# Optimization experiments

Hardware: AMD Instinct MI355X
Metric: run time of the kernel (lower is better)

## Reference

```python
import jax, jax.numpy as jnp
import numpy as np

S, N, A = 64, 4096, 32
HID, DM, NH, DK = 256, 128, 4, 32
EPS = 1e-5
SCALE = float(np.sqrt(DK))


def setup_inputs() -> dict:
    key = jax.random.key(0)
    ks = jax.random.split(key, 20)
    w = lambda i, sh: jax.random.normal(ks[i], sh, jnp.float32) * 0.02
    z = lambda n: jnp.zeros((n,), jnp.float32)
    return {
        "agent_states": jax.random.normal(ks[0], (N, S), jnp.float32),
        "sw1": w(1, (N * S, HID)), "sb1": z(HID),
        "sw2": w(2, (HID, HID)), "sb2": z(HID),
        "sow": w(3, (HID, 64)), "sob": z(64),
        "tw": w(4, (S + 64, DM)), "tb": z(DM),
        "wq": w(5, (DM, DM)), "bq": z(DM),
        "wk": w(6, (DM, DM)), "bk": z(DM),
        "wv": w(7, (DM, DM)), "bv": z(DM),
        "wo": w(8, (DM, DM)), "bo": z(DM),
        "ln_g": jnp.ones((DM,), jnp.float32), "ln_b": z(DM),
        "taw1": w(9, (DM, 64)), "tab1": z(64),
        "taw2": w(10, (64, 32)), "tab2": z(32),
        "ow1": w(11, (S + DM + 32, 256)), "ob1": z(256),
        "ow2": w(12, (256, DM)), "ob2": z(DM),
        "aw": w(13, (DM, A)), "ab": z(A),
        "vw": w(14, (DM, 1)), "vb": z(1),
        "cw": w(15, (S, 64)), "cb": z(64),
        "cdw": w(16, (64, 32)), "cdb": z(32),
    }


def reference(agent_states, sw1, sb1, sw2, sb2, sow, sob, tw, tb,
              wq, bq, wk, bk, wv, bv, wo, bo, ln_g, ln_b,
              taw1, tab1, taw2, tab2, ow1, ob1, ow2, ob2,
              aw, ab, vw, vb, cw, cb, cdw, cdb):
    n = agent_states.shape[0]
    # strategic level: flatten all agent states -> global objective [64]
    gs = agent_states.reshape(-1)
    strat = jax.nn.relu(jax.nn.relu(gs @ sw1 + sb1) @ sw2 + sb2)
    gobj = strat @ sow + sob
    # tactical encode (batched over agents instead of Python loop)
    tact_in = jnp.concatenate(
        [agent_states, jnp.broadcast_to(gobj, (n, gobj.shape[0]))], axis=-1)
    tact = jax.nn.relu(tact_in @ tw + tb)[None]  # [1, n, DM]
    # multi-head attention across agents
    q = (tact @ wq + bq).reshape(1, n, NH, DK).transpose(0, 2, 1, 3)
    k = (tact @ wk + bk).reshape(1, n, NH, DK).transpose(0, 2, 1, 3)
    v = (tact @ wv + bv).reshape(1, n, NH, DK).transpose(0, 2, 1, 3)
    scores = jnp.einsum('bhqd,bhkd->bhqk', q, k) / SCALE
    attn = jax.nn.softmax(scores, axis=-1)  # [1, NH, n, n]
    ctx = jnp.einsum('bhqk,bhkd->bhqd', attn, v).transpose(0, 2, 1, 3).reshape(1, n, DM)
    res = ctx @ wo + bo + tact
    mu = res.mean(-1, keepdims=True)
    var = res.var(-1, keepdims=True)  # biased, like torch LayerNorm
    coord = ((res - mu) / jnp.sqrt(var + EPS) * ln_g + ln_b)[0]  # [n, DM]
    # task allocation (softmax over 32 tasks)
    task = jax.nn.softmax(jax.nn.relu(coord @ taw1 + tab1) @ taw2 + tab2, axis=-1)
    # operational level -> actions / values
    op_in = jnp.concatenate([agent_states, coord, task], axis=-1)
    opf = jax.nn.relu(jax.nn.relu(op_in @ ow1 + ob1) @ ow2 + ob2)
    actions = opf @ aw + ab
    values = opf @ vw + vb
    # communication messages (two stacked linears, no activation in source)
    messages = (agent_states @ cw + cb) @ cdw + cdb
    return actions, values, messages, task, attn, gobj
```

## Files before the change

kernel.cpp:

```cpp
#include <hip/hip_runtime.h>

typedef __attribute__((ext_vector_type(8))) short s8v;
typedef __attribute__((ext_vector_type(4))) short s4v;
typedef __attribute__((ext_vector_type(4))) float f4v;

#define MFMA16(a, b, c) __builtin_amdgcn_mfma_f32_16x16x32_bf16((a), (b), (c), 0, 0, 0)

#define NAG   4096
#define SDIM  64
#define DMOD  128
#define NHD   4
#define DKD   32
#define HIDD  256
static constexpr float INV_SCALE = 0.17677669529663687f;
static constexpr float EPSV = 1e-5f;

#define OFF_ACT   0
#define OFF_VAL   131072
#define OFF_MSG   135168
#define OFF_TASK  266240
#define OFF_ATTN  397312
#define OFF_GOBJ  67506176

static constexpr size_t WS_P1   = 0;
static constexpr size_t WS_P1B  = 524288;
static constexpr size_t WS_P2   = 540672;
static constexpr size_t WS_TACT = 558080;
static constexpr size_t WS_Q    = 2655232;
static constexpr size_t WS_K    = 3703808;
static constexpr size_t WS_VT   = 4752384;
static constexpr size_t WS_CTX  = 5800960;
static constexpr size_t WS_OPIN = 7898112;
static constexpr size_t WS_H    = 9733120;
static constexpr size_t WS_OPF  = 11830272;
static constexpr size_t WS_OW1T = 12878848;
static constexpr size_t WS_OW2T = 12993536;

typedef unsigned short u16;
typedef unsigned int   u32;

static __device__ __forceinline__ u16 f2bf(float f) {
    union { float f; u32 u; } x; x.f = f;
    u32 r = x.u + 0x7FFFu + ((x.u >> 16) & 1u);
    return (u16)(r >> 16);
}
static __device__ __forceinline__ float bf2f(u16 b) {
    union { u32 u; float f; } x; x.u = ((u32)b) << 16;
    return x.f;
}

__global__ __launch_bounds__(256) void k1_sw1(const float* __restrict__ gs,
                                              const float* __restrict__ sw1,
                                              float* __restrict__ p1,
                                              const float* __restrict__ ow1,
                                              const float* __restrict__ ow2,
                                              u16* __restrict__ w1t,
                                              u16* __restrict__ w2t) {
    int tid = threadIdx.x;
    int b = blockIdx.x;
    if (b >= 512) {
        int bb = b - 512;
        if (bb < 224) {
            w1t[tid * 224 + bb] = f2bf(ow1[bb * 256 + tid]);
        } else if (tid < 128) {
            int k0 = (bb - 224) * 8;
#pragma unroll
            for (int kk = 0; kk < 8; ++kk) {
                int k = k0 + kk;
                w2t[tid * 256 + k] = f2bf(ow2[k * 128 + tid]);
            }
        }
        return;
    }
    __shared__ float gsl[512];
    __shared__ float red[4][256];
    gsl[tid]       = gs[b * 512 + tid];
    gsl[tid + 256] = gs[b * 512 + 256 + tid];
    __syncthreads();
    int t = tid & 63;
    int rg = tid >> 6;
    const f4v* w4 = (const f4v*)sw1;
    f4v acc = {0.f, 0.f, 0.f, 0.f};
    size_t rb = (size_t)b * 512;
#pragma unroll 4
    for (int r = rg; r < 512; r += 4) {
        float g = gsl[r];
        f4v w = __builtin_nontemporal_load(&w4[(rb + r) * 64 + t]);
        acc[0] += g * w[0]; acc[1] += g * w[1]; acc[2] += g * w[2]; acc[3] += g * w[3];
    }
    red[rg][4 * t + 0] = acc[0]; red[rg][4 * t + 1] = acc[1];
    red[rg][4 * t + 2] = acc[2]; red[rg][4 * t + 3] = acc[3];
    __syncthreads();
    float s = red[0][tid] + red[1][tid] + red[2][tid] + red[3][tid];
    p1[b * 256 + tid] = s;
}

__global__ void k1b_red(const float* __restrict__ p1, float* __restrict__ p1b) {
    int j = threadIdx.x;
    int b0 = blockIdx.x * 32;
    float s = 0.f;
#pragma unroll
    for (int b = 0; b < 32; ++b) s += p1[(b0 + b) * 256 + j];
    p1b[blockIdx.x * 256 + j] = s;
}

__global__ void k2b_strat(const float* __restrict__ p1b, const float* __restrict__ sb1,
                          const float* __restrict__ sw2, float* __restrict__ p2) {
    __shared__ float h1[256];
    int j = threadIdx.x;
    float s = 0.f;
#pragma unroll
    for (int b = 0; b < 16; ++b) s += p1b[b * 256 + j];
    h1[j] = fmaxf(s + sb1[j], 0.f);
    __syncthreads();
    int i0 = blockIdx.x * 16;
    float acc = 0.f;
#pragma unroll
    for (int i = 0; i < 16; ++i) acc += h1[i0 + i] * sw2[(i0 + i) * 256 + j];
    p2[blockIdx.x * 256 + j] = acc;
}

__global__ __launch_bounds__(256) void k3_tact_qkv(
    const float* __restrict__ p2, const float* __restrict__ sb2,
    const float* __restrict__ sow, const float* __restrict__ sob,
    const float* __restrict__ as, const float* __restrict__ tw, const float* __restrict__ tb,
    const float* __restrict__ wq, const float* __restrict__ bq,
    const float* __restrict__ wk, const float* __restrict__ bk,
    const float* __restrict__ wv, const float* __restrict__ bv,
    float* __restrict__ out_gobj, float* __restrict__ tactws,
    u16* __restrict__ qws, u16* __restrict__ kws, u16* __restrict__ vtws) {
    __shared__ float strat[256];
    __shared__ float gobj[64];
    __shared__ float asl[8][64];
    __shared__ float tl[8][128];
    int tid = threadIdx.x;
    int a0 = blockIdx.x * 8;
    {
        float s = 0.f;
#pragma unroll
        for (int b = 0; b < 16; ++b) s += p2[b * 256 + tid];
        strat[tid] = fmaxf(s + sb2[tid], 0.f);
    }
#pragma unroll
    for (int r = 0; r < 2; ++r) {
        int idx = tid + r * 256;
        asl[idx >> 6][idx & 63] = as[a0 * 64 + idx];
    }
    __syncthreads();
    if (tid < 64) {
        float g = sob[tid];
        for (int i = 0; i < 256; ++i) g += strat[i] * sow[i * 64 + tid];
        gobj[tid] = g;
        if (blockIdx.x == 0) out_gobj[tid] = g;
    }
    __syncthreads();
    int ah = tid >> 7, j = tid & 127;
    float gacc = 0.f;
    for (int i = 0; i < 64; ++i) gacc += gobj[i] * tw[(64 + i) * 128 + j];
    float acc[4];
    float base = tb[j] + gacc;
#pragma unroll
    for (int a = 0; a < 4; ++a) acc[a] = base;
    for (int i = 0; i < 64; ++i) {
        float w = tw[i * 128 + j];
#pragma unroll
        for (int a = 0; a < 4; ++a) acc[a] += asl[ah * 4 + a][i] * w;
    }
#pragma unroll
    for (int a = 0; a < 4; ++a) {
        float t = fmaxf(acc[a], 0.f);
        tl[ah * 4 + a][j] = t;
        tactws[(size_t)(a0 + ah * 4 + a) * 128 + j] = t;
    }
    __syncthreads();
    int h = j >> 5, d = j & 31;
#pragma unroll
    for (int a = 0; a < 4; ++a) acc[a] = 0.f;
    for (int i = 0; i < 128; ++i) {
        float w = wq[i * 128 + j];
#pragma unroll
        for (int a = 0; a < 4; ++a) acc[a] += tl[ah * 4 + a][i] * w;
    }
#pragma unroll
    for (int a = 0; a < 4; ++a)
        qws[h * 131072 + (a0 + ah * 4 + a) * 32 + d] = f2bf((acc[a] + bq[j]) * INV_SCALE);
#pragma unroll
    for (int a = 0; a < 4; ++a) acc[a] = 0.f;
    for (int i = 0; i < 128; ++i) {
        float w = wk[i * 128 + j];
#pragma unroll
        for (int a = 0; a < 4; ++a) acc[a] += tl[ah * 4 + a][i] * w;
    }
#pragma unroll
    for (int a = 0; a < 4; ++a)
        kws[h * 131072 + (a0 + ah * 4 + a) * 32 + d] = f2bf(acc[a] + bk[j]);
#pragma unroll
    for (int a = 0; a < 4; ++a) acc[a] = 0.f;
    for (int i = 0; i < 128; ++i) {
        float w = wv[i * 128 + j];
#pragma unroll
        for (int a = 0; a < 4; ++a) acc[a] += tl[ah * 4 + a][i] * w;
    }
    union { u16 u[4]; s4v v; } pk;
#pragma unroll
    for (int a = 0; a < 4; ++a) pk.u[a] = f2bf(acc[a] + bv[j]);
    *(s4v*)(vtws + h * 131072 + d * 4096 + a0 + ah * 4) = pk.v;
}

__global__ __launch_bounds__(512) void k4_attn(
    const u16* __restrict__ qws, const u16* __restrict__ kws, const u16* __restrict__ vtws,
    float* __restrict__ attn, float* __restrict__ ctxws) {
    int tid = threadIdx.x;
    int wid = tid >> 6;
    int l = tid & 63;
    int g = l >> 4;
    int ln = l & 15;
    int h = blockIdx.x >> 8;
    int qt = (blockIdx.x & 255) * 16;
    const u16* qh = qws + h * 131072;
    const u16* kh = kws + h * 131072;
    const u16* vh = vtws + h * 131072;
    int j0 = wid * 512;

    s8v aq = *(const s8v*)(qh + (qt + ln) * 32 + 8 * g);
    f4v zero = {0.f, 0.f, 0.f, 0.f};

    __shared__ __align__(16) union SmemU {
        struct {
            float red[8][16];
            u16 ldsPb[8][2][16][40];
            float pctx[8][16][32];
        } a;
        float sT[2][16][260];
    } sm;

    f4v lacc = zero, accA = zero, accB = zero;
    int buf = 0;
    for (int jc = 0; jc < 16; ++jc) {
        int jb = j0 + jc * 32;
        s8v b0 = *(const s8v*)(kh + (jb + ln) * 32 + 8 * g);
        s8v b1 = *(const s8v*)(kh + (jb + 16 + ln) * 32 + 8 * g);
        f4v S0 = MFMA16(aq, b0, zero);
        f4v S1 = MFMA16(aq, b1, zero);
#pragma unroll
        for (int r = 0; r < 4; ++r) {
            float w0 = __expf(S0[r]);
            float w1 = __expf(S1[r]);
            lacc[r] += w0 + w1;
            sm.a.ldsPb[wid][buf][4 * g + r][ln] = f2bf(w0);
            sm.a.ldsPb[wid][buf][4 * g + r][16 + ln] = f2bf(w1);
        }
        s8v bp = *(const s8v*)&sm.a.ldsPb[wid][buf][ln][8 * g];
        s8v va = *(const s8v*)(vh + ln * 4096 + jb + 8 * g);
        s8v vb = *(const s8v*)(vh + (16 + ln) * 4096 + jb + 8 * g);
        accA = MFMA16(va, bp, accA);
        accB = MFMA16(vb, bp, accB);
        buf ^= 1;
    }
#pragma unroll
    for (int m = 1; m <= 8; m <<= 1) {
        lacc[0] += __shfl_xor(lacc[0], m);
        lacc[1] += __shfl_xor(lacc[1], m);
        lacc[2] += __shfl_xor(lacc[2], m);
        lacc[3] += __shfl_xor(lacc[3], m);
    }
    if (ln == 0) {
#pragma unroll
        for (int r = 0; r < 4; ++r) sm.a.red[wid][4 * g + r] = lacc[r];
    }
    __syncthreads();
    float linvq = 1.f / (sm.a.red[0][ln] + sm.a.red[1][ln] + sm.a.red[2][ln] + sm.a.red[3][ln] +
                         sm.a.red[4][ln] + sm.a.red[5][ln] + sm.a.red[6][ln] + sm.a.red[7][ln]);
#pragma unroll
    for (int r = 0; r < 4; ++r) {
        sm.a.pctx[wid][ln][4 * g + r] = accA[r] * linvq;
        sm.a.pctx[wid][ln][16 + 4 * g + r] = accB[r] * linvq;
    }
    __syncthreads();
    {
        int q = tid >> 5;
        int d = tid & 31;
        float s = sm.a.pctx[0][q][d] + sm.a.pctx[1][q][d] + sm.a.pctx[2][q][d] + sm.a.pctx[3][q][d] +
                  sm.a.pctx[4][q][d] + sm.a.pctx[5][q][d] + sm.a.pctx[6][q][d] + sm.a.pctx[7][q][d];
        ctxws[(size_t)(qt + q) * 128 + h * 32 + d] = s;
    }
    __syncthreads();

    float* attnh = attn + (size_t)h * 4096 * 4096;
    auto COMPUTE = [&](int c, int p) {
        int co = wid * 32;
        int jb = c * 256 + co;
        s8v b0 = *(const s8v*)(kh + (jb + ln) * 32 + 8 * g);
        s8v b1 = *(const s8v*)(kh + (jb + 16 + ln) * 32 + 8 * g);
        f4v S0 = MFMA16(b0, aq, zero);
        f4v S1 = MFMA16(b1, aq, zero);
        f4v o0, o1;
#pragma unroll
        for (int r = 0; r < 4; ++r) {
            o0[r] = __expf(S0[r]) * linvq;
            o1[r] = __expf(S1[r]) * linvq;
        }
        *(f4v*)&sm.sT[p][ln][co + 4 * g] = o0;
        *(f4v*)&sm.sT[p][ln][co + 16 + 4 * g] = o1;
    };
    auto STORE = [&](int c, int p) {
#pragma unroll
        for (int r2 = 0; r2 < 2; ++r2) {
            int row = 2 * wid + r2;
            f4v t = *(const f4v*)&sm.sT[p][row][4 * l];
            *(f4v*)(attnh + (size_t)(qt + row) * 4096 + c * 256 + 4 * l) = t;
        }
    };
    COMPUTE(0, 0);
    __syncthreads();
    for (int c = 1; c < 16; ++c) {
        STORE(c - 1, (c - 1) & 1);
        COMPUTE(c, c & 1);
        __syncthreads();
    }
    STORE(15, 1);
}

__global__ __launch_bounds__(512) void k5_post(
    const float* __restrict__ ctxws, const float* __restrict__ tactws,
    const float* __restrict__ wo, const float* __restrict__ bo,
    const float* __restrict__ lng, const float* __restrict__ lnb,
    const float* __restrict__ taw1, const float* __restrict__ tab1,
    const float* __restrict__ taw2, const float* __restrict__ tab2,
    const float* __restrict__ as, float* __restrict__ dout, u16* __restrict__ opin) {
    __shared__ float wos[128 * 128];
    __shared__ float tw1s[128 * 64];
    __shared__ float tw2s[64 * 32];
    __shared__ float cx[8][128];
    __shared__ float coords[8][128];
    __shared__ float t1v[8][64];
    int tid = threadIdx.x;
    for (int i = tid; i < 128 * 128; i += 512) wos[i] = wo[i];
    for (int i = tid; i < 128 * 64; i += 512) tw1s[i] = taw1[i];
    for (int i = tid; i < 64 * 32; i += 512) tw2s[i] = taw2[i];
    __syncthreads();
    int w = tid >> 6, l = tid & 63;
    for (int it = 0; it < 2; ++it) {
        int n = blockIdx.x * 16 + w * 2 + it;
        float c0 = ctxws[(size_t)n * 128 + l], c1 = ctxws[(size_t)n * 128 + 64 + l];
        float t0 = tactws[(size_t)n * 128 + l], t1 = tactws[(size_t)n * 128 + 64 + l];
        float av = as[n * 64 + l];
        cx[w][l] = c0; cx[w][64 + l] = c1;
        __syncthreads();
        float r0 = bo[l] + t0, r1 = bo[64 + l] + t1;
        for (int k = 0; k < 128; ++k) {
            float cv = cx[w][k];
            r0 += cv * wos[k * 128 + l];
            r1 += cv * wos[k * 128 + 64 + l];
        }
        float s = r0 + r1;
#pragma unroll
        for (int m = 1; m <= 32; m <<= 1) s += __shfl_xor(s, m);
        float mu = s * (1.f / 128.f);
        float d0 = r0 - mu, d1 = r1 - mu;
        float vs = d0 * d0 + d1 * d1;
#pragma unroll
        for (int m = 1; m <= 32; m <<= 1) vs += __shfl_xor(vs, m);
        float rstd = 1.f / sqrtf(vs * (1.f / 128.f) + EPSV);
        float co0 = d0 * rstd * lng[l] + lnb[l];
        float co1 = d1 * rstd * lng[64 + l] + lnb[64 + l];
        coords[w][l] = co0; coords[w][64 + l] = co1;
        opin[(size_t)n * 224 + l] = f2bf(av);
        opin[(size_t)n * 224 + 64 + l] = f2bf(co0);
        opin[(size_t)n * 224 + 128 + l] = f2bf(co1);
        __syncthreads();
        float a1 = tab1[l];
        for (int i = 0; i < 128; ++i) a1 += coords[w][i] * tw1s[i * 64 + l];
        t1v[w][l] = fmaxf(a1, 0.f);
        __syncthreads();
        if (l < 32) {
            float a2 = tab2[l];
            for (int i = 0; i < 64; ++i) a2 += t1v[w][i] * tw2s[i * 32 + l];
            float mx = a2;
#pragma unroll
            for (int m = 1; m <= 16; m <<= 1) mx = fmaxf(mx, __shfl_xor(mx, m));
            float e = __expf(a2 - mx);
            float se = e;
#pragma unroll
            for (int m = 1; m <= 16; m <<= 1) se += __shfl_xor(se, m);
            float tk = e / se;
            dout[OFF_TASK + n * 32 + l] = tk;
            opin[(size_t)n * 224 + 192 + l] = f2bf(tk);
        }
        __syncthreads();
    }
}

__global__ __launch_bounds__(256) void k6a(const u16* __restrict__ opin, const u16* __restrict__ w1t,
                                           const float* __restrict__ ob1, u16* __restrict__ Hws) {
    int tid = threadIdx.x;
    int w = tid >> 6, l = tid & 63, g = l >> 4, ln = l & 15;
    int bm = blockIdx.x & 63, bn = blockIdx.x >> 6;
    int m0 = bm * 64 + w * 16, n0 = bn * 64;
    f4v acc[4];
    f4v zero = {0.f, 0.f, 0.f, 0.f};
#pragma unroll
    for (int nt = 0; nt < 4; ++nt) acc[nt] = zero;
    for (int kt = 0; kt < 7; ++kt) {
        s8v A = *(const s8v*)(opin + (size_t)(m0 + ln) * 224 + kt * 32 + 8 * g);
#pragma unroll
        for (int nt = 0; nt < 4; ++nt) {
            s8v B = *(const s8v*)(w1t + (size_t)(n0 + nt * 16 + ln) * 224 + kt * 32 + 8 * g);
            acc[nt] = MFMA16(A, B, acc[nt]);
        }
    }
#pragma unroll
    for (int nt = 0; nt < 4; ++nt) {
        int col = n0 + nt * 16 + ln;
        float bias = ob1[col];
#pragma unroll
        for (int r = 0; r < 4; ++r) {
            int row = m0 + 4 * g + r;
            Hws[(size_t)row * 256 + col] = f2bf(fmaxf(acc[nt][r] + bias, 0.f));
        }
    }
}

__global__ __launch_bounds__(256) void k6b(const u16* __restrict__ Hws, const u16* __restrict__ w2t,
                                           const float* __restrict__ ob2, u16* __restrict__ opfws) {
    int tid = threadIdx.x;
    int w = tid >> 6, l = tid & 63, g = l >> 4, ln = l & 15;
    int bm = blockIdx.x & 63, bn = blockIdx.x >> 6;
    int m0 = bm * 64 + w * 16, n0 = bn * 64;
    f4v acc[4];
    f4v zero = {0.f, 0.f, 0.f, 0.f};
#pragma unroll
    for (int nt = 0; nt < 4; ++nt) acc[nt] = zero;
    for (int kt = 0; kt < 8; ++kt) {
        s8v A = *(const s8v*)(Hws + (size_t)(m0 + ln) * 256 + kt * 32 + 8 * g);
#pragma unroll
        for (int nt = 0; nt < 4; ++nt) {
            s8v B = *(const s8v*)(w2t + (size_t)(n0 + nt * 16 + ln) * 256 + kt * 32 + 8 * g);
            acc[nt] = MFMA16(A, B, acc[nt]);
        }
    }
#pragma unroll
    for (int nt = 0; nt < 4; ++nt) {
        int col = n0 + nt * 16 + ln;
        float bias = ob2[col];
#pragma unroll
        for (int r = 0; r < 4; ++r) {
            int row = m0 + 4 * g + r;
            opfws[(size_t)row * 128 + col] = f2bf(fmaxf(acc[nt][r] + bias, 0.f));
        }
    }
}

__global__ __launch_bounds__(256) void k6c(const u16* __restrict__ opf, const float* __restrict__ as,
                                           const float* __restrict__ aw, const float* __restrict__ ab,
                                           const float* __restrict__ vw, const float* __restrict__ vb,
                                           const float* __restrict__ cw, const float* __restrict__ cb,
                                           const float* __restrict__ cdw, const float* __restrict__ cdb,
                                           float* __restrict__ dout) {
    __shared__ float opfs[4][128];
    __shared__ float asl[4][64];
    __shared__ float m1s[4][64];
    int tid = threadIdx.x;
    int w = tid >> 6, l = tid & 63;
    int n = blockIdx.x * 4 + w;
    {
        u32 u = *(const u32*)(opf + (size_t)n * 128 + 2 * l);
        opfs[w][2 * l] = bf2f((u16)(u & 0xffff));
        opfs[w][2 * l + 1] = bf2f((u16)(u >> 16));
        asl[w][l] = as[n * 64 + l];
    }
    __syncthreads();
    if (l < 32) {
        float a = ab[l];
        for (int k = 0; k < 128; ++k) a += opfs[w][k] * aw[k * 32 + l];
        dout[OFF_ACT + n * 32 + l] = a;
    }
    {
        float p = opfs[w][l] * vw[l] + opfs[w][64 + l] * vw[64 + l];
#pragma unroll
        for (int m = 1; m <= 32; m <<= 1) p += __shfl_xor(p, m);
        if (l == 0) dout[OFF_VAL + n] = p + vb[0];
    }
    {
        float a = cb[l];
        for (int k = 0; k < 64; ++k) a += asl[w][k] * cw[k * 64 + l];
        m1s[w][l] = a;
    }
    __syncthreads();
    if (l < 32) {
        float a = cdb[l];
        for (int k = 0; k < 64; ++k) a += m1s[w][k] * cdw[k * 32 + l];
        dout[OFF_MSG + n * 32 + l] = a;
    }
}

extern "C" void kernel_launch(void* const* d_in, const int* in_sizes, int n_in,
                              void* d_out, int out_size, void* d_ws, size_t ws_size,
                              hipStream_t stream) {
    const float* as  = (const float*)d_in[0];
    const float* sw1 = (const float*)d_in[1];
    const float* sb1 = (const float*)d_in[2];
    const float* sw2 = (const float*)d_in[3];
    const float* sb2 = (const float*)d_in[4];
    const float* sow = (const float*)d_in[5];
    const float* sob = (const float*)d_in[6];
    const float* tw  = (const float*)d_in[7];
    const float* tb  = (const float*)d_in[8];
    const float* wq  = (const float*)d_in[9];
    const float* bq  = (const float*)d_in[10];
    const float* wk  = (const float*)d_in[11];
    const float* bk  = (const float*)d_in[12];
    const float* wv  = (const float*)d_in[13];
    const float* bv  = (const float*)d_in[14];
    const float* wo  = (const float*)d_in[15];
    const float* bo  = (const float*)d_in[16];
    const float* lng = (const float*)d_in[17];
    const float* lnb = (const float*)d_in[18];
    const float* taw1 = (const float*)d_in[19];
    const float* tab1 = (const float*)d_in[20];
    const float* taw2 = (const float*)d_in[21];
    const float* tab2 = (const float*)d_in[22];
    const float* ow1 = (const float*)d_in[23];
    const float* ob1 = (const float*)d_in[24];
    const float* ow2 = (const float*)d_in[25];
    const float* ob2 = (const float*)d_in[26];
    const float* aw  = (const float*)d_in[27];
    const float* ab  = (const float*)d_in[28];
    const float* vw  = (const float*)d_in[29];
    const float* vb  = (const float*)d_in[30];
    const float* cw  = (const float*)d_in[31];
    const float* cb  = (const float*)d_in[32];
    const float* cdw = (const float*)d_in[33];
    const float* cdb = (const float*)d_in[34];

    float* dout = (float*)d_out;
    char* ws = (char*)d_ws;
    float* p1    = (float*)(ws + WS_P1);
    float* p1b   = (float*)(ws + WS_P1B);
    float* p2    = (float*)(ws + WS_P2);
    float* tactw = (float*)(ws + WS_TACT);
    u16*   qws   = (u16*)(ws + WS_Q);
    u16*   kws   = (u16*)(ws + WS_K);
    u16*   vtws  = (u16*)(ws + WS_VT);
    float* ctxws = (float*)(ws + WS_CTX);
    u16*   opin  = (u16*)(ws + WS_OPIN);
    u16*   Hws   = (u16*)(ws + WS_H);
    u16*   opfws = (u16*)(ws + WS_OPF);
    u16*   w1t   = (u16*)(ws + WS_OW1T);
    u16*   w2t   = (u16*)(ws + WS_OW2T);

    hipLaunchKernelGGL(k1_sw1, dim3(768), dim3(256), 0, stream, as, sw1, p1, ow1, ow2, w1t, w2t);
    hipLaunchKernelGGL(k1b_red, dim3(16), dim3(256), 0, stream, p1, p1b);
    hipLaunchKernelGGL(k2b_strat, dim3(16), dim3(256), 0, stream, p1b, sb1, sw2, p2);
    hipLaunchKernelGGL(k3_tact_qkv, dim3(512), dim3(256), 0, stream,
                       p2, sb2, sow, sob, as, tw, tb, wq, bq, wk, bk, wv, bv,
                       dout + OFF_GOBJ, tactw, qws, kws, vtws);
    hipLaunchKernelGGL(k4_attn, dim3(1024), dim3(512), 0, stream,
                       qws, kws, vtws, dout + OFF_ATTN, ctxws);
    hipLaunchKernelGGL(k5_post, dim3(256), dim3(512), 0, stream,
                       ctxws, tactw, wo, bo, lng, lnb, taw1, tab1, taw2, tab2, as, dout, opin);
    hipLaunchKernelGGL(k6a, dim3(256), dim3(256), 0, stream, opin, w1t, ob1, Hws);
    hipLaunchKernelGGL(k6b, dim3(128), dim3(256), 0, stream, Hws, w2t, ob2, opfws);
    hipLaunchKernelGGL(k6c, dim3(1024), dim3(256), 0, stream,
                       opfws, as, aw, ab, vw, vb, cw, cb, cdw, cdb, dout);
}
```

Measured before the change: 194.5 us.

## Fuse operational GEMM2 with action/value/message heads; drop LDS weight staging in k5

The second operational GEMM and the action, value and message head kernel are merged into one kernel. Each block now computes a full 64x128 opf tile, keeps it in shared memory as fp32, and runs register-blocked head matmuls on it. This removes the bf16 opf round-trip through global memory and one kernel launch, but cuts the grid to 64 blocks. Separately, k5_post no longer copies wo, taw1 and taw2 into about 96KB of shared memory. It reads them through the cache instead and drops block-wide barriers, since each wave only uses its own shared rows. That should raise occupancy and remove the per-block staging cost.

```diff
diff --git a/kernel.cpp b/kernel.cpp
--- a/kernel.cpp
+++ b/kernel.cpp
@@ -328,17 +328,10 @@
     const float* __restrict__ taw1, const float* __restrict__ tab1,
     const float* __restrict__ taw2, const float* __restrict__ tab2,
     const float* __restrict__ as, float* __restrict__ dout, u16* __restrict__ opin) {
-    __shared__ float wos[128 * 128];
-    __shared__ float tw1s[128 * 64];
-    __shared__ float tw2s[64 * 32];
     __shared__ float cx[8][128];
     __shared__ float coords[8][128];
     __shared__ float t1v[8][64];
     int tid = threadIdx.x;
-    for (int i = tid; i < 128 * 128; i += 512) wos[i] = wo[i];
-    for (int i = tid; i < 128 * 64; i += 512) tw1s[i] = taw1[i];
-    for (int i = tid; i < 64 * 32; i += 512) tw2s[i] = taw2[i];
-    __syncthreads();
     int w = tid >> 6, l = tid & 63;
     for (int it = 0; it < 2; ++it) {
         int n = blockIdx.x * 16 + w * 2 + it;
@@ -346,12 +339,11 @@
         float t0 = tactws[(size_t)n * 128 + l], t1 = tactws[(size_t)n * 128 + 64 + l];
         float av = as[n * 64 + l];
         cx[w][l] = c0; cx[w][64 + l] = c1;
-        __syncthreads();
         float r0 = bo[l] + t0, r1 = bo[64 + l] + t1;
         for (int k = 0; k < 128; ++k) {
             float cv = cx[w][k];
-            r0 += cv * wos[k * 128 + l];
-            r1 += cv * wos[k * 128 + 64 + l];
+            r0 += cv * wo[k * 128 + l];
+            r1 += cv * wo[k * 128 + 64 + l];
         }
         float s = r0 + r1;
 #pragma unroll
@@ -368,14 +360,12 @@
         opin[(size_t)n * 224 + l] = f2bf(av);
         opin[(size_t)n * 224 + 64 + l] = f2bf(co0);
         opin[(size_t)n * 224 + 128 + l] = f2bf(co1);
-        __syncthreads();
         float a1 = tab1[l];
-        for (int i = 0; i < 128; ++i) a1 += coords[w][i] * tw1s[i * 64 + l];
+        for (int i = 0; i < 128; ++i) a1 += coords[w][i] * taw1[i * 64 + l];
         t1v[w][l] = fmaxf(a1, 0.f);
-        __syncthreads();
         if (l < 32) {
             float a2 = tab2[l];
-            for (int i = 0; i < 64; ++i) a2 += t1v[w][i] * tw2s[i * 32 + l];
+            for (int i = 0; i < 64; ++i) a2 += t1v[w][i] * taw2[i * 32 + l];
             float mx = a2;
 #pragma unroll
             for (int m = 1; m <= 16; m <<= 1) mx = fmaxf(mx, __shfl_xor(mx, m));
@@ -387,7 +377,6 @@
             dout[OFF_TASK + n * 32 + l] = tk;
             opin[(size_t)n * 224 + 192 + l] = f2bf(tk);
         }
-        __syncthreads();
     }
 }
 
@@ -421,76 +410,92 @@
     }
 }
 
-__global__ __launch_bounds__(256) void k6b(const u16* __restrict__ Hws, const u16* __restrict__ w2t,
-                                           const float* __restrict__ ob2, u16* __restrict__ opfws) {
+__global__ __launch_bounds__(256) void k6bc(const u16* __restrict__ Hws, const u16* __restrict__ w2t,
+                                            const float* __restrict__ ob2, const float* __restrict__ as,
+                                            const float* __restrict__ aw, const float* __restrict__ ab,
+                                            const float* __restrict__ vw, const float* __restrict__ vb,
+                                            const float* __restrict__ cw, const float* __restrict__ cb,
+                                            const float* __restrict__ cdw, const float* __restrict__ cdb,
+                                            float* __restrict__ dout) {
+    __shared__ float opfs[64][128];
+    __shared__ float asl[64][64];
+    __shared__ float m1s[64][64];
     int tid = threadIdx.x;
     int w = tid >> 6, l = tid & 63, g = l >> 4, ln = l & 15;
-    int bm = blockIdx.x & 63, bn = blockIdx.x >> 6;
-    int m0 = bm * 64 + w * 16, n0 = bn * 64;
-    f4v acc[4];
+    int m0 = blockIdx.x * 64;
+    int mw = m0 + w * 16;
+    for (int i = tid; i < 64 * 64; i += 256) asl[i >> 6][i & 63] = as[m0 * 64 + i];
+    f4v acc[8];
     f4v zero = {0.f, 0.f, 0.f, 0.f};
 #pragma unroll
-    for (int nt = 0; nt < 4; ++nt) acc[nt] = zero;
+    for (int nt = 0; nt < 8; ++nt) acc[nt] = zero;
     for (int kt = 0; kt < 8; ++kt) {
-        s8v A = *(const s8v*)(Hws + (size_t)(m0 + ln) * 256 + kt * 32 + 8 * g);
-#pragma unroll
-        for (int nt = 0; nt < 4; ++nt) {
-            s8v B = *(const s8v*)(w2t + (size_t)(n0 + nt * 16 + ln) * 256 + kt * 32 + 8 * g);
+        s8v A = *(const s8v*)(Hws + (size_t)(mw + ln) * 256 + kt * 32 + 8 * g);
+#pragma unroll
+        for (int nt = 0; nt < 8; ++nt) {
+            s8v B = *(const s8v*)(w2t + (size_t)(nt * 16 + ln) * 256 + kt * 32 + 8 * g);
             acc[nt] = MFMA16(A, B, acc[nt]);
         }
     }
 #pragma unroll
-    for (int nt = 0; nt < 4; ++nt) {
-        int col = n0 + nt * 16 + ln;
+    for (int nt = 0; nt < 8; ++nt) {
+        int col = nt * 16 + ln;
         float bias = ob2[col];
 #pragma unroll
-        for (int r = 0; r < 4; ++r) {
-            int row = m0 + 4 * g + r;
-            opfws[(size_t)row * 128 + col] = f2bf(fmaxf(acc[nt][r] + bias, 0.f));
-        }
-    }
-}
-
-__global__ __launch_bounds__(256) void k6c(const u16* __restrict__ opf, const float* __restrict__ as,
-                                           const float* __restrict__ aw, const float* __restrict__ ab,
-                                           const float* __restrict__ vw, const float* __restrict__ vb,
-                                           const float* __restrict__ cw, const float* __restrict__ cb,
-                                           const float* __restrict__ cdw, const float* __restrict__ cdb,
-                                           float* __restrict__ dout) {
-    __shared__ float opfs[4][128];
-    __shared__ float asl[4][64];
-    __shared__ float m1s[4][64];
-    int tid = threadIdx.x;
-    int w = tid >> 6, l = tid & 63;
-    int n = blockIdx.x * 4 + w;
+        for (int r = 0; r < 4; ++r)
+            opfs[w * 16 + 4 * g + r][col] = fmaxf(acc[nt][r] + bias, 0.f);
+    }
+    __syncthreads();
     {
-        u32 u = *(const u32*)(opf + (size_t)n * 128 + 2 * l);
-        opfs[w][2 * l] = bf2f((u16)(u & 0xffff));
-        opfs[w][2 * l + 1] = bf2f((u16)(u >> 16));
-        asl[w][l] = as[n * 64 + l];
-    }
-    __syncthreads();
-    if (l < 32) {
-        float a = ab[l];
-        for (int k = 0; k < 128; ++k) a += opfs[w][k] * aw[k * 32 + l];
-        dout[OFF_ACT + n * 32 + l] = a;
+        int c = tid & 31;
+        int r0 = (tid >> 5) * 8;
+        float o[8];
+#pragma unroll
+        for (int r = 0; r < 8; ++r) o[r] = ab[c];
+        for (int k = 0; k < 128; ++k) {
+            float wv_ = aw[k * 32 + c];
+#pragma unroll
+            for (int r = 0; r < 8; ++r) o[r] += opfs[r0 + r][k] * wv_;
+        }
+#pragma unroll
+        for (int r = 0; r < 8; ++r) dout[OFF_ACT + (m0 + r0 + r) * 32 + c] = o[r];
     }
     {
-        float p = opfs[w][l] * vw[l] + opfs[w][64 + l] * vw[64 + l];
-#pragma unroll
-        for (int m = 1; m <= 32; m <<= 1) p += __shfl_xor(p, m);
-        if (l == 0) dout[OFF_VAL + n] = p + vb[0];
+        int r = tid >> 2, q = tid & 3;
+        float p = 0.f;
+        for (int k = q * 32; k < q * 32 + 32; ++k) p += opfs[r][k] * vw[k];
+        p += __shfl_xor(p, 1);
+        p += __shfl_xor(p, 2);
+        if (q == 0) dout[OFF_VAL + m0 + r] = p + vb[0];
     }
     {
-        float a = cb[l];
-        for (int k = 0; k < 64; ++k) a += asl[w][k] * cw[k * 64 + l];
-        m1s[w][l] = a;
-    }
-    __syncthreads();
-    if (l < 32) {
-        float a = cdb[l];
-        for (int k = 0; k < 64; ++k) a += m1s[w][k] * cdw[k * 32 + l];
-        dout[OFF_MSG + n * 32 + l] = a;
+        int j = tid & 63;
+        int r0 = (tid >> 6) * 16;
+        float mo[16];
+#pragma unroll
+        for (int r = 0; r < 16; ++r) mo[r] = cb[j];
+        for (int k = 0; k < 64; ++k) {
+            float wv_ = cw[k * 64 + j];
+#pragma unroll
+            for (int r = 0; r < 16; ++r) mo[r] += asl[r0 + r][k] * wv_;
+        }
+#pragma unroll
+        for (int r = 0; r < 16; ++r) m1s[r0 + r][j] = mo[r];
+    }
+    __syncthreads();
+    {
+        int c = tid & 31;
+        int r0 = (tid >> 5) * 8;
+        float o[8];
+#pragma unroll
+        for (int r = 0; r < 8; ++r) o[r] = cdb[c];
+        for (int k = 0; k < 64; ++k) {
+            float wv_ = cdw[k * 32 + c];
+#pragma unroll
+            for (int r = 0; r < 8; ++r) o[r] += m1s[r0 + r][k] * wv_;
+        }
+#pragma unroll
+        for (int r = 0; r < 8; ++r) dout[OFF_MSG + (m0 + r0 + r) * 32 + c] = o[r];
     }
 }
 
@@ -545,7 +550,6 @@
     float* ctxws = (float*)(ws + WS_CTX);
     u16*   opin  = (u16*)(ws + WS_OPIN);
     u16*   Hws   = (u16*)(ws + WS_H);
-    u16*   opfws = (u16*)(ws + WS_OPF);
     u16*   w1t   = (u16*)(ws + WS_OW1T);
     u16*   w2t   = (u16*)(ws + WS_OW2T);
 
@@ -560,7 +564,6 @@
     hipLaunchKernelGGL(k5_post, dim3(256), dim3(512), 0, stream,
                        ctxws, tactw, wo, bo, lng, lnb, taw1, tab1, taw2, tab2, as, dout, opin);
     hipLaunchKernelGGL(k6a, dim3(256), dim3(256), 0, stream, opin, w1t, ob1, Hws);
-    hipLaunchKernelGGL(k6b, dim3(128), dim3(256), 0, stream, Hws, w2t, ob2, opfws);
-    hipLaunchKernelGGL(k6c, dim3(1024), dim3(256), 0, stream,
-                       opfws, as, aw, ab, vw, vb, cw, cb, cdw, cdb, dout);
-}
+    hipLaunchKernelGGL(k6bc, dim3(64), dim3(256), 0, stream,
+                       Hws, w2t, ob2, as, aw, ab, vw, vb, cw, cb, cdw, cdb, dout);
+}
```

New measurement: 297.4 us. 52.9% more time.
